# Kernel tuning notes

Measured on AMD Instinct MI355X. Metric: run time of the kernel, lower is better.

Reference implementation:

```python
import jax, jax.numpy as jnp
import numpy as np

N_NODES = 100000
N_EDGES = 1600000
N_GRAPHS = 256
F_IN, F_HID, F_OUT = 32, 64, 64


def setup_inputs() -> dict:
    key = jax.random.key(0)
    ks = jax.random.split(key, 9)
    x = jax.random.normal(ks[0], (N_NODES, F_IN), dtype=jnp.float32)
    edge_index = jax.random.randint(ks[1], (2, N_EDGES), 0, N_NODES, dtype=jnp.int64)
    batch = jnp.sort(jax.random.randint(ks[2], (N_NODES,), 0, N_GRAPHS, dtype=jnp.int64))
    def glorot(k, fan_in, fan_out):
        lim = (6.0 / (fan_in + fan_out)) ** 0.5
        return jax.random.uniform(k, (fan_in, fan_out), jnp.float32, -lim, lim)
    return {
        "x": x,
        "edge_index": edge_index,
        "batch": batch,
        # GraphConv layer 1: lin_rel (with bias) on aggregated msgs, lin_root (no bias) on self
        "W1_rel": glorot(ks[3], F_IN, F_HID),
        "b1_rel": jnp.zeros((F_HID,), jnp.float32),
        "W1_root": glorot(ks[4], F_IN, F_HID),
        # GraphConv layer 2
        "W2_rel": glorot(ks[5], F_HID, F_OUT),
        "b2_rel": jnp.zeros((F_OUT,), jnp.float32),
        "W2_root": glorot(ks[6], F_HID, F_OUT),
    }


def _graph_conv(h, src, dst, W_rel, b_rel, W_root):
    # PyG GraphConv (aggr='add'): out_i = W_rel @ (sum_{j->i} h_j) + b_rel + W_root @ h_i
    agg = jax.ops.segment_sum(h[src], dst, num_segments=N_NODES)  # [N, F]
    return agg @ W_rel + b_rel + h @ W_root


def reference(x, edge_index, batch, W1_rel, b1_rel, W1_root, W2_rel, b2_rel, W2_root):
    src, dst = edge_index[0], edge_index[1]
    h1 = jnp.tanh(_graph_conv(x, src, dst, W1_rel, b1_rel, W1_root))   # [N, 64]
    h2 = jnp.tanh(_graph_conv(h1, src, dst, W2_rel, b2_rel, W2_root))  # [N, 64]
    # global_mean_pool over graph ids
    sums = jax.ops.segment_sum(h2, batch, num_segments=N_GRAPHS)       # [B, 64]
    counts = jax.ops.segment_sum(jnp.ones((h2.shape[0],), h2.dtype), batch, num_segments=N_GRAPHS)
    return sums / jnp.maximum(counts, 1.0)[:, None]
```

## Files before the change

### kernel.cpp

```cpp
#include <hip/hip_runtime.h>

#define N_NODES 100000
#define N_EDGES 1600000
#define N_GRAPHS 256
#define F_IN 32
#define F_HID 64
#define F_OUT 64

#define T_WAVES 2048
#define NODES_PER_WAVE ((N_NODES + T_WAVES - 1) / T_WAVES)

__global__ void histogram_dst(const int* __restrict__ dst, int* __restrict__ deg) {
    int e = blockIdx.x * blockDim.x + threadIdx.x;
    if (e < N_EDGES) atomicAdd(&deg[dst[e]], 1);
}

__global__ void scan1(const int* __restrict__ deg, int* __restrict__ end_, int* __restrict__ partials) {
    __shared__ int s[256];
    int tid = threadIdx.x;
    int i = blockIdx.x * 256 + tid;
    int v = (i < N_NODES) ? deg[i] : 0;
    s[tid] = v;
    __syncthreads();
#pragma unroll
    for (int off = 1; off < 256; off <<= 1) {
        int t = 0;
        if (tid >= off) t = s[tid - off];
        __syncthreads();
        if (tid >= off) s[tid] += t;
        __syncthreads();
    }
    if (i < N_NODES) end_[i] = s[tid];
    if (tid == 255) partials[blockIdx.x] = s[255];
}

__global__ void scan2(int* __restrict__ partials, int nb) {
    __shared__ int s[512];
    int tid = threadIdx.x;
    int v = (tid < nb) ? partials[tid] : 0;
    s[tid] = v;
    __syncthreads();
#pragma unroll
    for (int off = 1; off < 512; off <<= 1) {
        int t = 0;
        if (tid >= off) t = s[tid - off];
        __syncthreads();
        if (tid >= off) s[tid] += t;
        __syncthreads();
    }
    int excl = (tid > 0) ? s[tid - 1] : 0;
    if (tid < nb) partials[tid] = excl;
}

__global__ void scan3(const int* __restrict__ deg, int* __restrict__ end_,
                      int* __restrict__ cursor, const int* __restrict__ partials) {
    int i = blockIdx.x * 256 + threadIdx.x;
    if (i < N_NODES) {
        int e = end_[i] + partials[blockIdx.x];
        end_[i] = e;
        cursor[i] = e - deg[i];
    }
}

__global__ void fill_adj(const int* __restrict__ src, const int* __restrict__ dst,
                         int* __restrict__ cursor, int* __restrict__ adj) {
    int e = blockIdx.x * blockDim.x + threadIdx.x;
    if (e < N_EDGES) {
        int d = dst[e];
        int pos = atomicAdd(&cursor[d], 1);
        adj[pos] = src[e];
    }
}

__global__ __launch_bounds__(256) void gather64(const float* __restrict__ h,
        const int* __restrict__ adj, const int* __restrict__ end_, const int* __restrict__ deg,
        float* __restrict__ agg) {
    int wid = (blockIdx.x * blockDim.x + threadIdx.x) >> 6;
    int lane = threadIdx.x & 63;
    if (wid >= N_NODES) return;
    int e = end_[wid];
    int d = deg[wid];
    int s = e - d;
    float acc = 0.0f;
    for (int base = 0; base < d; base += 64) {
        int chunk = min(64, d - base);
        int myadj = (base + lane < d) ? adj[s + base + lane] : 0;
        int j = 0;
        for (; j + 4 <= chunk; j += 4) {
            int s0 = __shfl(myadj, j);
            int s1 = __shfl(myadj, j + 1);
            int s2 = __shfl(myadj, j + 2);
            int s3 = __shfl(myadj, j + 3);
            float v0 = h[(size_t)s0 * 64 + lane];
            float v1 = h[(size_t)s1 * 64 + lane];
            float v2 = h[(size_t)s2 * 64 + lane];
            float v3 = h[(size_t)s3 * 64 + lane];
            acc += v0 + v1 + v2 + v3;
        }
        for (; j < chunk; ++j) {
            int sn = __shfl(myadj, j);
            acc += h[(size_t)sn * 64 + lane];
        }
    }
    agg[(size_t)wid * 64 + lane] = acc;
}

__global__ __launch_bounds__(256) void gather32(const float* __restrict__ xin,
        const int* __restrict__ adj, const int* __restrict__ end_, const int* __restrict__ deg,
        float* __restrict__ agg) {
    int wid = (blockIdx.x * blockDim.x + threadIdx.x) >> 6;
    int lane = threadIdx.x & 63;
    int hw = lane >> 5;
    int f = lane & 31;
    int node = wid * 2 + hw;
    if (node >= N_NODES) return;
    int e = end_[node];
    int d = deg[node];
    int s = e - d;
    float acc = 0.0f;
    for (int base = 0; base < d; base += 32) {
        int chunk = min(32, d - base);
        int myadj = (base + f < d) ? adj[s + base + f] : 0;
        int j = 0;
        for (; j + 4 <= chunk; j += 4) {
            int s0 = __shfl(myadj, hw * 32 + j);
            int s1 = __shfl(myadj, hw * 32 + j + 1);
            int s2 = __shfl(myadj, hw * 32 + j + 2);
            int s3 = __shfl(myadj, hw * 32 + j + 3);
            float v0 = xin[(size_t)s0 * 32 + f];
            float v1 = xin[(size_t)s1 * 32 + f];
            float v2 = xin[(size_t)s2 * 32 + f];
            float v3 = xin[(size_t)s3 * 32 + f];
            acc += v0 + v1 + v2 + v3;
        }
        for (; j < chunk; ++j) {
            int sn = __shfl(myadj, hw * 32 + j);
            acc += xin[(size_t)sn * 32 + f];
        }
    }
    agg[(size_t)node * 32 + f] = acc;
}

__global__ __launch_bounds__(256) void transform1_reg(const float* __restrict__ agg,
        const float* __restrict__ xin,
        const float* __restrict__ Wrel, const float* __restrict__ brel,
        const float* __restrict__ Wroot,
        float* __restrict__ h1) {
    int lane = threadIdx.x & 63;
    int wgid = __builtin_amdgcn_readfirstlane(blockIdx.x * 4 + (threadIdx.x >> 6));
    int n0 = wgid * NODES_PER_WAVE;
    if (n0 >= N_NODES) return;
    int n1 = min(n0 + NODES_PER_WAVE, N_NODES);

    float wrel[32], wroot[32];
#pragma unroll
    for (int k = 0; k < 32; ++k) {
        wrel[k] = Wrel[k * 64 + lane];
        wroot[k] = Wroot[k * 64 + lane];
    }
    float b = brel[lane];

    for (int node = n0; node < n1; ++node) {
        const float4* ar = (const float4*)(agg + (size_t)node * 32);
        const float4* xr = (const float4*)(xin + (size_t)node * 32);
        float o = b;
#pragma unroll
        for (int kk = 0; kk < 8; ++kk) {
            float4 a4 = ar[kk];
            float4 x4 = xr[kk];
            o += a4.x * wrel[kk * 4 + 0] + a4.y * wrel[kk * 4 + 1]
               + a4.z * wrel[kk * 4 + 2] + a4.w * wrel[kk * 4 + 3];
            o += x4.x * wroot[kk * 4 + 0] + x4.y * wroot[kk * 4 + 1]
               + x4.z * wroot[kk * 4 + 2] + x4.w * wroot[kk * 4 + 3];
        }
        h1[(size_t)node * 64 + lane] = tanhf(o);
    }
}

__global__ __launch_bounds__(256) void transform2_pool_reg(const float* __restrict__ agg,
        const float* __restrict__ h1,
        const float* __restrict__ Wrel, const float* __restrict__ brel,
        const float* __restrict__ Wroot,
        const int* __restrict__ batch,
        float* __restrict__ sums) {
    int lane = threadIdx.x & 63;
    int wgid = __builtin_amdgcn_readfirstlane(blockIdx.x * 4 + (threadIdx.x >> 6));
    int n0 = wgid * NODES_PER_WAVE;
    if (n0 >= N_NODES) return;
    int n1 = min(n0 + NODES_PER_WAVE, N_NODES);

    float wrel[64], wroot[64];
#pragma unroll
    for (int k = 0; k < 64; ++k) {
        wrel[k] = Wrel[k * 64 + lane];
        wroot[k] = Wroot[k * 64 + lane];
    }
    float b = brel[lane];

    float psum = 0.0f;
    int curg = batch[n0];
    for (int node = n0; node < n1; ++node) {
        const float4* ar = (const float4*)(agg + (size_t)node * 64);
        const float4* xr = (const float4*)(h1 + (size_t)node * 64);
        float o = b;
#pragma unroll
        for (int kk = 0; kk < 16; ++kk) {
            float4 a4 = ar[kk];
            float4 x4 = xr[kk];
            o += a4.x * wrel[kk * 4 + 0] + a4.y * wrel[kk * 4 + 1]
               + a4.z * wrel[kk * 4 + 2] + a4.w * wrel[kk * 4 + 3];
            o += x4.x * wroot[kk * 4 + 0] + x4.y * wroot[kk * 4 + 1]
               + x4.z * wroot[kk * 4 + 2] + x4.w * wroot[kk * 4 + 3];
        }
        float h2 = tanhf(o);
        int g = batch[node];
        if (g != curg) {
            atomicAdd(&sums[(size_t)curg * 64 + lane], psum);
            psum = 0.0f;
            curg = g;
        }
        psum += h2;
    }
    atomicAdd(&sums[(size_t)curg * 64 + lane], psum);
}

__global__ void graph_counts(const int* __restrict__ batch, float* __restrict__ counts) {
    int g = threadIdx.x;
    if (g >= N_GRAPHS) return;
    int lo = 0, hi = N_NODES;
    while (lo < hi) { int mid = (lo + hi) >> 1; if (batch[mid] < g) lo = mid + 1; else hi = mid; }
    int start = lo;
    lo = 0; hi = N_NODES;
    while (lo < hi) { int mid = (lo + hi) >> 1; if (batch[mid] <= g) lo = mid + 1; else hi = mid; }
    counts[g] = (float)(lo - start);
}

__global__ void finalize(const float* __restrict__ sums,
                         const float* __restrict__ counts,
                         float* __restrict__ out) {
    int i = blockIdx.x * blockDim.x + threadIdx.x;
    if (i < N_GRAPHS * 64) {
        float c = counts[i >> 6];
        out[i] = sums[i] / fmaxf(c, 1.0f);
    }
}

extern "C" void kernel_launch(void* const* d_in, const int* in_sizes, int n_in,
                              void* d_out, int out_size, void* d_ws, size_t ws_size,
                              hipStream_t stream) {
    const float* x       = (const float*)d_in[0];
    const int*   ei      = (const int*)d_in[1];
    const int*   batch   = (const int*)d_in[2];
    const float* W1_rel  = (const float*)d_in[3];
    const float* b1_rel  = (const float*)d_in[4];
    const float* W1_root = (const float*)d_in[5];
    const float* W2_rel  = (const float*)d_in[6];
    const float* b2_rel  = (const float*)d_in[7];
    const float* W2_root = (const float*)d_in[8];
    float* out = (float*)d_out;

    const int* src = ei;
    const int* dst = ei + N_EDGES;

    char* ws = (char*)d_ws;
    int*   deg      = (int*)(ws + 0);
    float* sums     = (float*)(ws + 400000);
    float* counts   = (float*)(ws + 465536);
    int*   end_     = (int*)(ws + 466560);
    int*   cursor   = (int*)(ws + 866560);
    int*   partials = (int*)(ws + 1266560);
    int*   adj      = (int*)(ws + 1268608);
    float* aggbuf   = (float*)(ws + 7668608);
    float* h1       = (float*)(ws + 33268608);

    hipMemsetAsync(d_ws, 0, 466560, stream);

    const int NB_NODE = (N_NODES + 255) / 256;
    histogram_dst<<<(N_EDGES + 255) / 256, 256, 0, stream>>>(dst, deg);
    scan1<<<NB_NODE, 256, 0, stream>>>(deg, end_, partials);
    scan2<<<1, 512, 0, stream>>>(partials, NB_NODE);
    scan3<<<NB_NODE, 256, 0, stream>>>(deg, end_, cursor, partials);
    fill_adj<<<(N_EDGES + 255) / 256, 256, 0, stream>>>(src, dst, cursor, adj);

    gather32<<<((N_NODES + 1) / 2 * 64 + 255) / 256, 256, 0, stream>>>(x, adj, end_, deg, aggbuf);
    transform1_reg<<<T_WAVES / 4, 256, 0, stream>>>(aggbuf, x, W1_rel, b1_rel, W1_root, h1);

    gather64<<<(N_NODES * 64 + 255) / 256, 256, 0, stream>>>(h1, adj, end_, deg, aggbuf);
    transform2_pool_reg<<<T_WAVES / 4, 256, 0, stream>>>(aggbuf, h1, W2_rel, b2_rel, W2_root, batch, sums);

    graph_counts<<<1, 256, 0, stream>>>(batch, counts);
    finalize<<<(N_GRAPHS * 64 + 255) / 256, 256, 0, stream>>>(sums, counts, out);
}
```

Measured before the change: 431.4 us.

## Bucket CSR fill by destination range and vectorize neighbor gathers with float4

The CSR fill now makes several passes over the edge list, and each pass only scatters edges whose destination falls in a 16K-node window. This keeps the atomic cursor updates and adjacency writes within a small, cache-friendly region, at the cost of reading dst about seven times. Both gather kernels now use one wavefront per node, with lanes split into float4 feature slices across several neighbors at once. Partial sums are reduced with xor shuffles. This raises memory-level parallelism and uses wider loads, but it idles part of the wave for low-degree nodes and gather32 now launches twice the waves.

```diff
diff --git a/kernel.cpp b/kernel.cpp
--- a/kernel.cpp
+++ b/kernel.cpp
@@ -9,6 +9,8 @@
 
 #define T_WAVES 2048
 #define NODES_PER_WAVE ((N_NODES + T_WAVES - 1) / T_WAVES)
+#define FILL_PASS_SHIFT 14
+#define FILL_NPASS ((N_NODES + (1 << FILL_PASS_SHIFT) - 1) >> FILL_PASS_SHIFT)
 
 __global__ void histogram_dst(const int* __restrict__ dst, int* __restrict__ deg) {
     int e = blockIdx.x * blockDim.x + threadIdx.x;
@@ -62,83 +64,103 @@
     }
 }
 
-__global__ void fill_adj(const int* __restrict__ src, const int* __restrict__ dst,
-                         int* __restrict__ cursor, int* __restrict__ adj) {
-    int e = blockIdx.x * blockDim.x + threadIdx.x;
-    if (e < N_EDGES) {
-        int d = dst[e];
-        int pos = atomicAdd(&cursor[d], 1);
-        adj[pos] = src[e];
-    }
-}
-
-__global__ __launch_bounds__(256) void gather64(const float* __restrict__ h,
+__global__ __launch_bounds__(256) void fill_adj_mp(const int* __restrict__ src,
+                                                   const int* __restrict__ dst,
+                                                   int* __restrict__ cursor,
+                                                   int* __restrict__ adj) {
+    int gid = blockIdx.x * blockDim.x + threadIdx.x;
+    int stride = gridDim.x * blockDim.x;
+    for (int p = 0; p < FILL_NPASS; ++p) {
+        for (int e = gid; e < N_EDGES; e += stride) {
+            int d = dst[e];
+            if ((d >> FILL_PASS_SHIFT) == p) {
+                int pos = atomicAdd(&cursor[d], 1);
+                adj[pos] = src[e];
+            }
+        }
+    }
+}
+
+__global__ __launch_bounds__(256) void gather64_v2(const float* __restrict__ h,
         const int* __restrict__ adj, const int* __restrict__ end_, const int* __restrict__ deg,
         float* __restrict__ agg) {
-    int wid = (blockIdx.x * blockDim.x + threadIdx.x) >> 6;
+    int node = (blockIdx.x * blockDim.x + threadIdx.x) >> 6;
     int lane = threadIdx.x & 63;
-    if (wid >= N_NODES) return;
-    int e = end_[wid];
-    int d = deg[wid];
-    int s = e - d;
-    float acc = 0.0f;
-    for (int base = 0; base < d; base += 64) {
-        int chunk = min(64, d - base);
-        int myadj = (base + lane < d) ? adj[s + base + lane] : 0;
-        int j = 0;
-        for (; j + 4 <= chunk; j += 4) {
-            int s0 = __shfl(myadj, j);
-            int s1 = __shfl(myadj, j + 1);
-            int s2 = __shfl(myadj, j + 2);
-            int s3 = __shfl(myadj, j + 3);
-            float v0 = h[(size_t)s0 * 64 + lane];
-            float v1 = h[(size_t)s1 * 64 + lane];
-            float v2 = h[(size_t)s2 * 64 + lane];
-            float v3 = h[(size_t)s3 * 64 + lane];
-            acc += v0 + v1 + v2 + v3;
-        }
-        for (; j < chunk; ++j) {
-            int sn = __shfl(myadj, j);
-            acc += h[(size_t)sn * 64 + lane];
-        }
-    }
-    agg[(size_t)wid * 64 + lane] = acc;
-}
-
-__global__ __launch_bounds__(256) void gather32(const float* __restrict__ xin,
-        const int* __restrict__ adj, const int* __restrict__ end_, const int* __restrict__ deg,
-        float* __restrict__ agg) {
-    int wid = (blockIdx.x * blockDim.x + threadIdx.x) >> 6;
-    int lane = threadIdx.x & 63;
-    int hw = lane >> 5;
-    int f = lane & 31;
-    int node = wid * 2 + hw;
     if (node >= N_NODES) return;
     int e = end_[node];
     int d = deg[node];
     int s = e - d;
-    float acc = 0.0f;
-    for (int base = 0; base < d; base += 32) {
-        int chunk = min(32, d - base);
-        int myadj = (base + f < d) ? adj[s + base + f] : 0;
-        int j = 0;
-        for (; j + 4 <= chunk; j += 4) {
-            int s0 = __shfl(myadj, hw * 32 + j);
-            int s1 = __shfl(myadj, hw * 32 + j + 1);
-            int s2 = __shfl(myadj, hw * 32 + j + 2);
-            int s3 = __shfl(myadj, hw * 32 + j + 3);
-            float v0 = xin[(size_t)s0 * 32 + f];
-            float v1 = xin[(size_t)s1 * 32 + f];
-            float v2 = xin[(size_t)s2 * 32 + f];
-            float v3 = xin[(size_t)s3 * 32 + f];
-            acc += v0 + v1 + v2 + v3;
-        }
-        for (; j < chunk; ++j) {
-            int sn = __shfl(myadj, hw * 32 + j);
-            acc += xin[(size_t)sn * 32 + f];
-        }
-    }
-    agg[(size_t)node * 32 + f] = acc;
+    int q = lane & 15;
+    int r = lane >> 4;
+    const float4* h4 = (const float4*)h;
+
+    float ax = 0.f, ay = 0.f, az = 0.f, aw = 0.f;
+    for (int base = 0; base < d; base += 8) {
+        int i0 = base + r;
+        int i1 = base + 4 + r;
+        if (i0 < d) {
+            int s0 = adj[s + i0];
+            float4 v = h4[(size_t)s0 * 16 + q];
+            ax += v.x; ay += v.y; az += v.z; aw += v.w;
+        }
+        if (i1 < d) {
+            int s1 = adj[s + i1];
+            float4 v = h4[(size_t)s1 * 16 + q];
+            ax += v.x; ay += v.y; az += v.z; aw += v.w;
+        }
+    }
+#pragma unroll
+    for (int off = 16; off < 64; off <<= 1) {
+        ax += __shfl_xor(ax, off);
+        ay += __shfl_xor(ay, off);
+        az += __shfl_xor(az, off);
+        aw += __shfl_xor(aw, off);
+    }
+    if (r == 0) {
+        float4 o; o.x = ax; o.y = ay; o.z = az; o.w = aw;
+        ((float4*)agg)[(size_t)node * 16 + q] = o;
+    }
+}
+
+__global__ __launch_bounds__(256) void gather32_v2(const float* __restrict__ xin,
+        const int* __restrict__ adj, const int* __restrict__ end_, const int* __restrict__ deg,
+        float* __restrict__ agg) {
+    int node = (blockIdx.x * blockDim.x + threadIdx.x) >> 6;
+    int lane = threadIdx.x & 63;
+    if (node >= N_NODES) return;
+    int e = end_[node];
+    int d = deg[node];
+    int s = e - d;
+    int q = lane & 7;
+    int r = lane >> 3;
+    const float4* x4 = (const float4*)xin;
+
+    float ax = 0.f, ay = 0.f, az = 0.f, aw = 0.f;
+    for (int base = 0; base < d; base += 16) {
+        int i0 = base + r;
+        int i1 = base + 8 + r;
+        if (i0 < d) {
+            int s0 = adj[s + i0];
+            float4 v = x4[(size_t)s0 * 8 + q];
+            ax += v.x; ay += v.y; az += v.z; aw += v.w;
+        }
+        if (i1 < d) {
+            int s1 = adj[s + i1];
+            float4 v = x4[(size_t)s1 * 8 + q];
+            ax += v.x; ay += v.y; az += v.z; aw += v.w;
+        }
+    }
+#pragma unroll
+    for (int off = 8; off < 64; off <<= 1) {
+        ax += __shfl_xor(ax, off);
+        ay += __shfl_xor(ay, off);
+        az += __shfl_xor(az, off);
+        aw += __shfl_xor(aw, off);
+    }
+    if (r == 0) {
+        float4 o; o.x = ax; o.y = ay; o.z = az; o.w = aw;
+        ((float4*)agg)[(size_t)node * 8 + q] = o;
+    }
 }
 
 __global__ __launch_bounds__(256) void transform1_reg(const float* __restrict__ agg,
@@ -280,12 +302,12 @@
     scan1<<<NB_NODE, 256, 0, stream>>>(deg, end_, partials);
     scan2<<<1, 512, 0, stream>>>(partials, NB_NODE);
     scan3<<<NB_NODE, 256, 0, stream>>>(deg, end_, cursor, partials);
-    fill_adj<<<(N_EDGES + 255) / 256, 256, 0, stream>>>(src, dst, cursor, adj);
-
-    gather32<<<((N_NODES + 1) / 2 * 64 + 255) / 256, 256, 0, stream>>>(x, adj, end_, deg, aggbuf);
+    fill_adj_mp<<<2048, 256, 0, stream>>>(src, dst, cursor, adj);
+
+    gather32_v2<<<(N_NODES * 64 + 255) / 256, 256, 0, stream>>>(x, adj, end_, deg, aggbuf);
     transform1_reg<<<T_WAVES / 4, 256, 0, stream>>>(aggbuf, x, W1_rel, b1_rel, W1_root, h1);
 
-    gather64<<<(N_NODES * 64 + 255) / 256, 256, 0, stream>>>(h1, adj, end_, deg, aggbuf);
+    gather64_v2<<<(N_NODES * 64 + 255) / 256, 256, 0, stream>>>(h1, adj, end_, deg, aggbuf);
     transform2_pool_reg<<<T_WAVES / 4, 256, 0, stream>>>(aggbuf, h1, W2_rel, b2_rel, W2_root, batch, sums);
 
     graph_counts<<<1, 256, 0, stream>>>(batch, counts);
```

New measurement: 413.7 us. 4.1% less time.
